# Optimization experiments

Measured on AMD Instinct MI355X. Metric: run time of the kernel, lower is better.

Reference implementation:

```python
import jax, jax.numpy as jnp
import numpy as np

NUM_LAYERS = 2
HIDDEN = 512


def _lstm_layer(x_tbh, h0, c0, Wih, Whh, bih, bhh):
    """Run one LSTM layer over time.
    x_tbh: [T,B,I]; h0,c0: [B,H]; Wih: [4H,I]; Whh: [4H,H]; bih,bhh: [4H].
    Gate order follows torch.nn.LSTMCell: i, f, g, o.
    Returns (outputs [T,B,H], (h_T, c_T)).
    """
    bias = bih + bhh

    def step(carry, x_t):
        h, c = carry
        gates = x_t @ Wih.T + h @ Whh.T + bias  # [B,4H]
        i, f, g, o = jnp.split(gates, 4, axis=-1)
        i = jax.nn.sigmoid(i)
        f = jax.nn.sigmoid(f)
        g = jnp.tanh(g)
        o = jax.nn.sigmoid(o)
        c_new = f * c + i * g
        h_new = o * jnp.tanh(c_new)
        return (h_new, c_new), h_new

    (h_T, c_T), outs = jax.lax.scan(step, (h0, c0), x_tbh)
    return outs, (h_T, c_T)


def setup_inputs() -> dict:
    key = jax.random.key(0)
    ks = jax.random.split(key, 7)
    B, T, I, H, L = 32, 1024, 512, HIDDEN, NUM_LAYERS
    scale = 1.0 / np.sqrt(H)
    return {
        "input": jax.random.normal(ks[0], (B, T, I), dtype=jnp.float32),
        "h0": jax.random.normal(ks[1], (L, B, H), dtype=jnp.float32),
        "c0": jax.random.normal(ks[2], (L, B, H), dtype=jnp.float32),
        "W_ih": jax.random.normal(ks[3], (L, 4 * H, I), dtype=jnp.float32) * scale,
        "W_hh": jax.random.normal(ks[4], (L, 4 * H, H), dtype=jnp.float32) * scale,
        "b_ih": jax.random.normal(ks[5], (L, 4 * H), dtype=jnp.float32) * scale,
        "b_hh": jax.random.normal(ks[6], (L, 4 * H), dtype=jnp.float32) * scale,
    }


def reference(input, h0, c0, W_ih, W_hh, b_ih, b_hh):
    # batch_first=True -> transpose to time-major for the scan
    x = jnp.transpose(input, (1, 0, 2))  # [T,B,I]
    h_outs, c_outs = [], []
    for l in range(NUM_LAYERS):
        x, (h_T, c_T) = _lstm_layer(x, h0[l], c0[l], W_ih[l], W_hh[l], b_ih[l], b_hh[l])
        h_outs.append(h_T)
        c_outs.append(c_T)
    out = jnp.transpose(x, (1, 0, 2))  # back to [B,T,H]
    return out, (jnp.stack(h_outs), jnp.stack(c_outs))
```

## Files before the change

### kernel.cpp

```cpp
#include <hip/hip_runtime.h>
#include <math.h>

#define T_STEPS 1024
#define BATCH   32
#define HID     512
#define G4      2048
#define NWG     128
#define WGL     64
#define JPW     8
#define FPAD    32
#define RD      8

#define WS_FLAGS 0
#define WS_H1    16384
#define WS_H2    278528
#define WS_XBF   344064

#define OUT_ELEMS (BATCH * T_STEPS * HID)
#define H_OFF OUT_ELEMS
#define C_OFF (OUT_ELEMS + 2 * BATCH * HID)

typedef __attribute__((ext_vector_type(8)))  short short8;
typedef __attribute__((ext_vector_type(16))) float f32x16;

__device__ __forceinline__ unsigned short f2bf(float f) {
    union { float f; unsigned u; } v; v.f = f;
    unsigned r = v.u + 0x7fffu + ((v.u >> 16) & 1u);
    return (unsigned short)(r >> 16);
}
__device__ __forceinline__ float sigm(float x)  { return 1.0f / (1.0f + __expf(-x)); }
__device__ __forceinline__ float ftanh(float x) { return 1.0f - 2.0f / (__expf(2.0f * x) + 1.0f); }

__device__ __forceinline__ short8 ld_llc(const void* p) {
    short8 r;
    asm volatile("global_load_dwordx4 %0, %1, off sc0 sc1" : "=v"(r) : "v"(p));
    return r;
}

__device__ __forceinline__ void g_arrive(unsigned* flags, int wg, unsigned epoch, int tid) {
    asm volatile("s_waitcnt vmcnt(0)" ::: "memory");
    __syncthreads();
    if (tid == 0)
        __hip_atomic_store(&flags[wg * FPAD], epoch, __ATOMIC_RELAXED, __HIP_MEMORY_SCOPE_AGENT);
}

__device__ __forceinline__ void poll_ge(const unsigned* p, unsigned epoch) {
    while (__hip_atomic_load(p, __ATOMIC_RELAXED, __HIP_MEMORY_SCOPE_AGENT) < epoch)
        __builtin_amdgcn_s_sleep(1);
}

__global__ void init_flags(unsigned* flags) {
    for (int i = threadIdx.x; i < NWG * FPAD; i += 256) flags[i] = 0u;
}

__global__ void __launch_bounds__(256, 1)
lstm_persist(const float* __restrict__ x_in,
             const float* __restrict__ h0,
             const float* __restrict__ c0,
             const float* __restrict__ Wih,
             const float* __restrict__ Whh,
             const float* __restrict__ bih,
             const float* __restrict__ bhh,
             float* __restrict__ out,
             unsigned char* __restrict__ ws,
             int use_xbf)
{
    __shared__ float gatebuf[4][BATCH][36];
    __shared__ float biasbuf[32];

    const int wg    = blockIdx.x;
    const int layer = (wg >= WGL) ? 1 : 0;
    const int wgl   = wg - layer * WGL;
    const int jbase = wgl * JPW;
    const int tid   = threadIdx.x;

    unsigned* flags = (unsigned*)(ws + WS_FLAGS);
    unsigned short* h1ring = (unsigned short*)(ws + WS_H1);
    unsigned short* h2ring = (unsigned short*)(ws + WS_H2);
    unsigned short* xbf    = (unsigned short*)(ws + WS_XBF);

    if (use_xbf) {
        const size_t total4 = (size_t)BATCH * T_STEPS * HID / 4;
        unsigned long long* dst = (unsigned long long*)xbf;
        for (size_t idx = (size_t)wg * 256 + tid; idx < total4; idx += (size_t)NWG * 256) {
            float4 v = *(const float4*)(x_in + idx * 4);
            unsigned long long pk = (unsigned long long)f2bf(v.x)
                                  | ((unsigned long long)f2bf(v.y) << 16)
                                  | ((unsigned long long)f2bf(v.z) << 32)
                                  | ((unsigned long long)f2bf(v.w) << 48);
            dst[idx] = pk;
        }
        __builtin_amdgcn_fence(__ATOMIC_RELEASE, "agent");
    }

    if (tid < 32) {
        const int g = tid >> 3, jloc = tid & 7;
        const int r = g * HID + jbase + jloc;
        biasbuf[tid] = bih[(size_t)layer * G4 + r] + bhh[(size_t)layer * G4 + r];
    }

    const int lane = tid & 63;
    const int wv   = tid >> 6;
    const int hi   = lane >> 5;
    const int l31  = lane & 31;
    const int kb   = (wv & 1) * 256;

    short8 bW[16];
    {
        const float* Wsel = ((wv < 2) ? Wih : Whh) + (size_t)layer * G4 * HID;
        const int r = (l31 >> 3) * HID + jbase + (l31 & 7);
        const float* wr = Wsel + (size_t)r * HID + kb + hi * 8;
        #pragma unroll
        for (int j = 0; j < 16; ++j) {
            float4 v0 = *(const float4*)(wr + j * 16);
            float4 v1 = *(const float4*)(wr + j * 16 + 4);
            short8 p;
            p[0]=(short)f2bf(v0.x); p[1]=(short)f2bf(v0.y); p[2]=(short)f2bf(v0.z); p[3]=(short)f2bf(v0.w);
            p[4]=(short)f2bf(v1.x); p[5]=(short)f2bf(v1.y); p[6]=(short)f2bf(v1.z); p[7]=(short)f2bf(v1.w);
            bW[j] = p;
        }
    }

    const int m  = tid >> 3;
    const int jl = tid & 7;
    const int jg = jbase + jl;

    float creg = c0[((size_t)layer * BATCH + m) * HID + jg];

    {
        unsigned hb = (unsigned)f2bf(h0[((size_t)layer * BATCH + m) * HID + jg]);
        unsigned ob = __shfl_xor(hb, 1);
        if ((tid & 1) == 0) {
            unsigned val = hb | (ob << 16);
            if (layer == 0) {
                unsigned* p = (unsigned*)(h1ring + ((size_t)7 * BATCH + m) * HID + (jg & ~1));
                __hip_atomic_store(p, val, __ATOMIC_RELAXED, __HIP_MEMORY_SCOPE_AGENT);
            } else {
                unsigned* p0 = (unsigned*)(h2ring + ((size_t)0 * BATCH + m) * HID + (jg & ~1));
                unsigned* p1 = (unsigned*)(h2ring + ((size_t)1 * BATCH + m) * HID + (jg & ~1));
                __hip_atomic_store(p0, val, __ATOMIC_RELAXED, __HIP_MEMORY_SCOPE_AGENT);
                __hip_atomic_store(p1, val, __ATOMIC_RELAXED, __HIP_MEMORY_SCOPE_AGENT);
            }
        }
    }

    g_arrive(flags, wg, 1u, tid);
    if (tid < NWG) poll_ge(flags + tid * FPAD, 1u);
    __syncthreads();
    __builtin_amdgcn_fence(__ATOMIC_ACQUIRE, "agent");

    const unsigned* fL0 = flags;
    const unsigned* fL1 = flags + WGL * FPAD;

    short8 afr[16];

#define PREFX(tt)                                                             \
    do {                                                                      \
        if (use_xbf) {                                                        \
            const short* bx = (const short*)xbf +                             \
                ((size_t)l31 * T_STEPS + (tt)) * HID + kb + hi * 8;           \
            _Pragma("unroll")                                                 \
            for (int j = 0; j < 16; ++j)                                      \
                afr[j] = *(const short8*)(bx + j * 16);                       \
        } else {                                                              \
            const float* fx = x_in +                                          \
                ((size_t)l31 * T_STEPS + (tt)) * HID + kb + hi * 8;           \
            _Pragma("unroll")                                                 \
            for (int j = 0; j < 16; ++j) {                                    \
                float4 v0 = *(const float4*)(fx + j * 16);                    \
                float4 v1 = *(const float4*)(fx + j * 16 + 4);                \
                short8 p;                                                     \
                p[0]=(short)f2bf(v0.x); p[1]=(short)f2bf(v0.y);               \
                p[2]=(short)f2bf(v0.z); p[3]=(short)f2bf(v0.w);               \
                p[4]=(short)f2bf(v1.x); p[5]=(short)f2bf(v1.y);               \
                p[6]=(short)f2bf(v1.z); p[7]=(short)f2bf(v1.w);               \
                afr[j] = p;                                                   \
            }                                                                 \
        }                                                                     \
    } while (0)

    if (layer == 0 && wv < 2) PREFX(0);

    const int SE = T_STEPS + 2;
    for (int s = 0; s <= SE; ++s) {
        const int t = (layer == 0) ? s : s - 2;
        const bool active = (t >= 0) && (t < T_STEPS);
        const bool last = (s == SE);
        float hv = 0.0f;

        if (active) {
            if (wv >= 2) {
                const unsigned short* ring = (layer == 0) ? h1ring : h2ring;
                const size_t slot = (layer == 0) ? (size_t)((s - 1) & 7)
                                                 : (size_t)((s + 1) & 1);
                const short* base = (const short*)ring +
                    (slot * BATCH + l31) * HID + kb + hi * 8;
                #pragma unroll
                for (int j = 0; j < 16; ++j) afr[j] = ld_llc(base + j * 16);
            }
            asm volatile("s_waitcnt vmcnt(0)" ::: "memory");
            __builtin_amdgcn_sched_barrier(0);

            f32x16 acc0, acc1;
            #pragma unroll
            for (int r = 0; r < 16; ++r) { acc0[r] = 0.f; acc1[r] = 0.f; }
            #pragma unroll
            for (int j = 0; j < 16; j += 2) {
                acc0 = __builtin_amdgcn_mfma_f32_32x32x16_bf16(afr[j],     bW[j],     acc0, 0, 0, 0);
                acc1 = __builtin_amdgcn_mfma_f32_32x32x16_bf16(afr[j + 1], bW[j + 1], acc1, 0, 0, 0);
            }
            #pragma unroll
            for (int r = 0; r < 16; ++r)
                gatebuf[wv][(r & 3) + 8 * (r >> 2) + 4 * hi][l31] = acc0[r] + acc1[r];
            __syncthreads();

            float gi = gatebuf[0][m][jl]      + gatebuf[1][m][jl]
                     + gatebuf[2][m][jl]      + gatebuf[3][m][jl]      + biasbuf[jl];
            float gf = gatebuf[0][m][8  + jl] + gatebuf[1][m][8  + jl]
                     + gatebuf[2][m][8  + jl] + gatebuf[3][m][8  + jl] + biasbuf[8  + jl];
            float gg = gatebuf[0][m][16 + jl] + gatebuf[1][m][16 + jl]
                     + gatebuf[2][m][16 + jl] + gatebuf[3][m][16 + jl] + biasbuf[16 + jl];
            float go = gatebuf[0][m][24 + jl] + gatebuf[1][m][24 + jl]
                     + gatebuf[2][m][24 + jl] + gatebuf[3][m][24 + jl] + biasbuf[24 + jl];
            float iv = sigm(gi), fv = sigm(gf), gv = ftanh(gg), ov = sigm(go);
            creg = fv * creg + iv * gv;
            hv = ov * ftanh(creg);

            {
                unsigned hb = (unsigned)f2bf(hv);
                unsigned ob = __shfl_xor(hb, 1);
                if ((tid & 1) == 0) {
                    unsigned val = hb | (ob << 16);
                    unsigned* p;
                    if (layer == 0)
                        p = (unsigned*)(h1ring + ((size_t)(s & 7) * BATCH + m) * HID + (jg & ~1));
                    else
                        p = (unsigned*)(h2ring + ((size_t)(s & 1) * BATCH + m) * HID + (jg & ~1));
                    __hip_atomic_store(p, val, __ATOMIC_RELAXED, __HIP_MEMORY_SCOPE_AGENT);
                }
            }
            if (t == T_STEPS - 1)
                out[H_OFF + ((size_t)layer * BATCH + m) * HID + jg] = hv;
        }

        if (!last) {
            g_arrive(flags, wg, (unsigned)(s + 2), tid);

            if (layer == 1) {
                if (active)
                    out[((size_t)m * T_STEPS + t) * HID + jg] = hv;
                if (wv < 2 && s >= 1 && s <= T_STEPS) {
                    poll_ge(fL0 + lane * FPAD, (unsigned)(s + 1));
                    const short* base = (const short*)h1ring +
                        ((size_t)((s - 1) & 7) * BATCH + l31) * HID + kb + hi * 8;
                    #pragma unroll
                    for (int j = 0; j < 16; ++j) afr[j] = ld_llc(base + j * 16);
                }
                if (wv == 3)
                    poll_ge(fL1 + lane * FPAD, (unsigned)(s + 2));
            } else {
                if (wv < 2 && active && t + 1 < T_STEPS) PREFX(t + 1);
                if (wv == 2 && s >= 7)
                    poll_ge(fL1 + lane * FPAD, (unsigned)(s - 3));
                if (wv == 3)
                    poll_ge(fL0 + lane * FPAD, (unsigned)(s + 2));
            }
            __syncthreads();
        }
    }

    out[C_OFF + ((size_t)layer * BATCH + m) * HID + jg] = creg;
#undef PREFX
}

extern "C" void kernel_launch(void* const* d_in, const int* in_sizes, int n_in,
                              void* d_out, int out_size, void* d_ws, size_t ws_size,
                              hipStream_t stream) {
    const float* x   = (const float*)d_in[0];
    const float* h0  = (const float*)d_in[1];
    const float* c0  = (const float*)d_in[2];
    const float* Wih = (const float*)d_in[3];
    const float* Whh = (const float*)d_in[4];
    const float* bih = (const float*)d_in[5];
    const float* bhh = (const float*)d_in[6];
    float* out = (float*)d_out;
    unsigned char* ws = (unsigned char*)d_ws;

    const size_t xbf_need = (size_t)WS_XBF + (size_t)BATCH * T_STEPS * HID * 2;
    int use_xbf = (ws_size >= xbf_need) ? 1 : 0;

    hipLaunchKernelGGL(init_flags, dim3(1), dim3(256), 0, stream, (unsigned*)ws);

    void* args[] = { (void*)&x, (void*)&h0, (void*)&c0, (void*)&Wih, (void*)&Whh,
                     (void*)&bih, (void*)&bhh, (void*)&out, (void*)&ws, (void*)&use_xbf };
    hipError_t e = hipLaunchCooperativeKernel((void*)lstm_persist, dim3(NWG), dim3(256),
                                              args, 0, stream);
    if (e != hipSuccess) {
        hipLaunchKernelGGL(lstm_persist, dim3(NWG), dim3(256), 0, stream,
                           x, h0, c0, Wih, Whh, bih, bhh, out, ws, use_xbf);
    }
}
```

Baseline: 4.267 ms.

## Replace per-step flag barriers with poisoned-slot data polling on hidden-state rings

```diff
diff --git a/kernel.cpp b/kernel.cpp
--- a/kernel.cpp
+++ b/kernel.cpp
@@ -9,12 +9,17 @@
 #define WGL     64
 #define JPW     8
 #define FPAD    32
-#define RD      8
+#define NSLOT   16
+
+#define RBYTES  (NSLOT * WGL * BATCH * 8 * 2)
 
 #define WS_FLAGS 0
 #define WS_H1    16384
-#define WS_H2    278528
-#define WS_XBF   344064
+#define WS_H2    (WS_H1 + RBYTES)
+#define WS_XBF   (WS_H2 + RBYTES)
+
+#define POIS16  0x7FC0
+#define POIS32  0x7FC07FC0u
 
 #define OUT_ELEMS (BATCH * T_STEPS * HID)
 #define H_OFF OUT_ELEMS
@@ -22,6 +27,7 @@
 
 typedef __attribute__((ext_vector_type(8)))  short short8;
 typedef __attribute__((ext_vector_type(16))) float f32x16;
+typedef __attribute__((ext_vector_type(4)))  unsigned int u32x4;
 
 __device__ __forceinline__ unsigned short f2bf(float f) {
     union { float f; unsigned u; } v; v.f = f;
@@ -36,12 +42,8 @@
     asm volatile("global_load_dwordx4 %0, %1, off sc0 sc1" : "=v"(r) : "v"(p));
     return r;
 }
-
-__device__ __forceinline__ void g_arrive(unsigned* flags, int wg, unsigned epoch, int tid) {
-    asm volatile("s_waitcnt vmcnt(0)" ::: "memory");
-    __syncthreads();
-    if (tid == 0)
-        __hip_atomic_store(&flags[wg * FPAD], epoch, __ATOMIC_RELAXED, __HIP_MEMORY_SCOPE_AGENT);
+__device__ __forceinline__ void st16_llc(void* p, u32x4 v) {
+    asm volatile("global_store_dwordx4 %0, %1, off sc0 sc1" :: "v"(p), "v"(v) : "memory");
 }
 
 __device__ __forceinline__ void poll_ge(const unsigned* p, unsigned epoch) {
@@ -49,8 +51,22 @@
         __builtin_amdgcn_s_sleep(1);
 }
 
-__global__ void init_flags(unsigned* flags) {
-    for (int i = threadIdx.x; i < NWG * FPAD; i += 256) flags[i] = 0u;
+__device__ __forceinline__ void publish_row(unsigned short* dst16, float hv, int tid) {
+    unsigned hb = (unsigned)f2bf(hv);
+    unsigned v0 = hb | (((unsigned)__shfl_xor((int)hb, 1)) << 16);
+    unsigned v1 = (unsigned)__shfl_xor((int)v0, 2);
+    unsigned v2 = (unsigned)__shfl_xor((int)v0, 4);
+    unsigned v3 = (unsigned)__shfl_xor((int)v1, 4);
+    if ((tid & 7) == 0) {
+        u32x4 pk = { v0, v1, v2, v3 };
+        st16_llc((void*)dst16, pk);
+    }
+}
+
+__global__ void init_ws(unsigned* w) {
+    const int total = 4096 + 2 * (RBYTES / 4);
+    for (int i = blockIdx.x * 256 + threadIdx.x; i < total; i += gridDim.x * 256)
+        w[i] = (i < 4096) ? 0u : POIS32;
 }
 
 __global__ void __launch_bounds__(256, 1)
@@ -128,29 +144,19 @@
     float creg = c0[((size_t)layer * BATCH + m) * HID + jg];
 
     {
-        unsigned hb = (unsigned)f2bf(h0[((size_t)layer * BATCH + m) * HID + jg]);
-        unsigned ob = __shfl_xor(hb, 1);
-        if ((tid & 1) == 0) {
-            unsigned val = hb | (ob << 16);
-            if (layer == 0) {
-                unsigned* p = (unsigned*)(h1ring + ((size_t)7 * BATCH + m) * HID + (jg & ~1));
-                __hip_atomic_store(p, val, __ATOMIC_RELAXED, __HIP_MEMORY_SCOPE_AGENT);
-            } else {
-                unsigned* p0 = (unsigned*)(h2ring + ((size_t)0 * BATCH + m) * HID + (jg & ~1));
-                unsigned* p1 = (unsigned*)(h2ring + ((size_t)1 * BATCH + m) * HID + (jg & ~1));
-                __hip_atomic_store(p0, val, __ATOMIC_RELAXED, __HIP_MEMORY_SCOPE_AGENT);
-                __hip_atomic_store(p1, val, __ATOMIC_RELAXED, __HIP_MEMORY_SCOPE_AGENT);
-            }
-        }
-    }
-
-    g_arrive(flags, wg, 1u, tid);
+        float h0v = h0[((size_t)layer * BATCH + m) * HID + jg];
+        unsigned short* ringw = (layer == 0) ? h1ring : h2ring;
+        unsigned short* dst = ringw + (((size_t)15 * WGL + wgl) * BATCH + m) * 8;
+        publish_row(dst, h0v, tid);
+    }
+
+    asm volatile("s_waitcnt vmcnt(0)" ::: "memory");
+    __syncthreads();
+    if (tid == 0)
+        __hip_atomic_store(&flags[wg * FPAD], 1u, __ATOMIC_RELAXED, __HIP_MEMORY_SCOPE_AGENT);
     if (tid < NWG) poll_ge(flags + tid * FPAD, 1u);
     __syncthreads();
     __builtin_amdgcn_fence(__ATOMIC_ACQUIRE, "agent");
-
-    const unsigned* fL0 = flags;
-    const unsigned* fL1 = flags + WGL * FPAD;
 
     short8 afr[16];
 
@@ -179,27 +185,45 @@
         }                                                                     \
     } while (0)
 
+#define POLL_FRAGS(rbase)                                                     \
+    do {                                                                      \
+        for (;;) {                                                            \
+            _Pragma("unroll")                                                 \
+            for (int j = 0; j < 16; ++j)                                      \
+                afr[j] = ld_llc((rbase) + j * 512);                           \
+            asm volatile("s_waitcnt vmcnt(0)" ::: "memory");                  \
+            int stale = 0;                                                    \
+            _Pragma("unroll")                                                 \
+            for (int j = 0; j < 16; ++j) {                                    \
+                stale |= ((unsigned short)afr[j][0] == (unsigned short)POIS16); \
+                stale |= ((unsigned short)afr[j][2] == (unsigned short)POIS16); \
+                stale |= ((unsigned short)afr[j][4] == (unsigned short)POIS16); \
+                stale |= ((unsigned short)afr[j][6] == (unsigned short)POIS16); \
+            }                                                                 \
+            if (!__any(stale)) break;                                         \
+        }                                                                     \
+        __builtin_amdgcn_sched_barrier(0);                                    \
+    } while (0)
+
     if (layer == 0 && wv < 2) PREFX(0);
 
-    const int SE = T_STEPS + 2;
+    const int SE = T_STEPS + 1;
     for (int s = 0; s <= SE; ++s) {
         const int t = (layer == 0) ? s : s - 2;
         const bool active = (t >= 0) && (t < T_STEPS);
-        const bool last = (s == SE);
         float hv = 0.0f;
 
         if (active) {
             if (wv >= 2) {
                 const unsigned short* ring = (layer == 0) ? h1ring : h2ring;
-                const size_t slot = (layer == 0) ? (size_t)((s - 1) & 7)
-                                                 : (size_t)((s + 1) & 1);
+                const int slot = (t + 15) & 15;
                 const short* base = (const short*)ring +
-                    (slot * BATCH + l31) * HID + kb + hi * 8;
-                #pragma unroll
-                for (int j = 0; j < 16; ++j) afr[j] = ld_llc(base + j * 16);
-            }
-            asm volatile("s_waitcnt vmcnt(0)" ::: "memory");
-            __builtin_amdgcn_sched_barrier(0);
+                    (((size_t)slot * WGL + (kb >> 3) + hi) * BATCH + l31) * 8;
+                POLL_FRAGS(base);
+            } else {
+                asm volatile("s_waitcnt vmcnt(0)" ::: "memory");
+                __builtin_amdgcn_sched_barrier(0);
+            }
 
             f32x16 acc0, acc1;
             #pragma unroll
@@ -227,50 +251,51 @@
             hv = ov * ftanh(creg);
 
             {
-                unsigned hb = (unsigned)f2bf(hv);
-                unsigned ob = __shfl_xor(hb, 1);
-                if ((tid & 1) == 0) {
-                    unsigned val = hb | (ob << 16);
-                    unsigned* p;
-                    if (layer == 0)
-                        p = (unsigned*)(h1ring + ((size_t)(s & 7) * BATCH + m) * HID + (jg & ~1));
-                    else
-                        p = (unsigned*)(h2ring + ((size_t)(s & 1) * BATCH + m) * HID + (jg & ~1));
-                    __hip_atomic_store(p, val, __ATOMIC_RELAXED, __HIP_MEMORY_SCOPE_AGENT);
-                }
+                unsigned short* ringw = (layer == 0) ? h1ring : h2ring;
+                unsigned short* dst = ringw +
+                    (((size_t)(t & 15) * WGL + wgl) * BATCH + m) * 8;
+                publish_row(dst, hv, tid);
             }
             if (t == T_STEPS - 1)
                 out[H_OFF + ((size_t)layer * BATCH + m) * HID + jg] = hv;
         }
 
-        if (!last) {
-            g_arrive(flags, wg, (unsigned)(s + 2), tid);
-
-            if (layer == 1) {
-                if (active)
-                    out[((size_t)m * T_STEPS + t) * HID + jg] = hv;
-                if (wv < 2 && s >= 1 && s <= T_STEPS) {
-                    poll_ge(fL0 + lane * FPAD, (unsigned)(s + 1));
-                    const short* base = (const short*)h1ring +
-                        ((size_t)((s - 1) & 7) * BATCH + l31) * HID + kb + hi * 8;
-                    #pragma unroll
-                    for (int j = 0; j < 16; ++j) afr[j] = ld_llc(base + j * 16);
-                }
-                if (wv == 3)
-                    poll_ge(fL1 + lane * FPAD, (unsigned)(s + 2));
-            } else {
-                if (wv < 2 && active && t + 1 < T_STEPS) PREFX(t + 1);
-                if (wv == 2 && s >= 7)
-                    poll_ge(fL1 + lane * FPAD, (unsigned)(s - 3));
-                if (wv == 3)
-                    poll_ge(fL0 + lane * FPAD, (unsigned)(s + 2));
-            }
-            __syncthreads();
-        }
+        asm volatile("s_waitcnt vmcnt(0)" ::: "memory");
+        __syncthreads();
+        if (layer == 1 && tid == 0)
+            __hip_atomic_store(&flags[wg * FPAD], (unsigned)(s + 2),
+                               __ATOMIC_RELAXED, __HIP_MEMORY_SCOPE_AGENT);
+
+        {
+            unsigned short* ringw = (layer == 0) ? h1ring : h2ring;
+            unsigned short* dst = ringw +
+                (((size_t)((t + 8) & 15) * WGL + wgl) * BATCH + m) * 8;
+            if ((tid & 7) == 0) {
+                u32x4 pz = { POIS32, POIS32, POIS32, POIS32 };
+                st16_llc((void*)dst, pz);
+            }
+        }
+
+        if (layer == 1) {
+            if (active)
+                out[((size_t)m * T_STEPS + t) * HID + jg] = hv;
+            if (wv < 2 && t + 1 >= 0 && t + 1 < T_STEPS) {
+                const int slot = (s + 15) & 15;
+                const short* base = (const short*)h1ring +
+                    (((size_t)slot * WGL + (kb >> 3) + hi) * BATCH + l31) * 8;
+                POLL_FRAGS(base);
+            }
+        } else {
+            if (wv < 2 && active && t + 1 < T_STEPS) PREFX(t + 1);
+            if (wv == 2 && s >= 3 && lane < WGL)
+                poll_ge(flags + (WGL + lane) * FPAD, (unsigned)(s - 2));
+        }
+        __syncthreads();
     }
 
     out[C_OFF + ((size_t)layer * BATCH + m) * HID + jg] = creg;
 #undef PREFX
+#undef POLL_FRAGS
 }
 
 extern "C" void kernel_launch(void* const* d_in, const int* in_sizes, int n_in,
@@ -289,7 +314,7 @@
     const size_t xbf_need = (size_t)WS_XBF + (size_t)BATCH * T_STEPS * HID * 2;
     int use_xbf = (ws_size >= xbf_need) ? 1 : 0;
 
-    hipLaunchKernelGGL(init_flags, dim3(1), dim3(256), 0, stream, (unsigned*)ws);
+    hipLaunchKernelGGL(init_ws, dim3(64), dim3(256), 0, stream, (unsigned*)ws);
 
     void* args[] = { (void*)&x, (void*)&h0, (void*)&c0, (void*)&Wih, (void*)&Whh,
                      (void*)&bih, (void*)&bhh, (void*)&out, (void*)&ws, (void*)&use_xbf };
```

Result: slower. 5.033 ms (+18.0%).
